# Kernel optimization log

Measured on AMD Instinct MI355X. Metric: run time of the kernel, lower is better.

The kernel has to match this reference:

```python
import jax, jax.numpy as jnp
import numpy as np

N = 50000      # nodes
E = 800000     # edges (before self-loops)
IN_DIM = 128
HID = 64
HEADS = 4
NEG_SLOPE = 0.2  # PyG GATConv default leaky-relu slope


def setup_inputs() -> dict:
    key = jax.random.key(0)
    ks = jax.random.split(key, 12)
    s = 0.05
    return {
        "x": jax.random.normal(ks[0], (N, IN_DIM), jnp.float32),
        "edge_index": jax.random.randint(ks[1], (2, E), 0, N, dtype=jnp.int64),
        "W1": jax.random.normal(ks[2], (IN_DIM, HEADS * HID), jnp.float32) * s,
        "att1_src": jax.random.normal(ks[3], (HEADS, HID), jnp.float32) * s,
        "att1_dst": jax.random.normal(ks[4], (HEADS, HID), jnp.float32) * s,
        "b1": jax.random.normal(ks[5], (HEADS * HID,), jnp.float32) * s,
        "W2": jax.random.normal(ks[6], (HEADS * HID, HID), jnp.float32) * s,
        "att2_src": jax.random.normal(ks[7], (1, HID), jnp.float32) * s,
        "att2_dst": jax.random.normal(ks[8], (1, HID), jnp.float32) * s,
        "b2": jax.random.normal(ks[9], (HID,), jnp.float32) * s,
        "Wc": jax.random.normal(ks[10], (HID, 2), jnp.float32) * s,
        "bc": jax.random.normal(ks[11], (2,), jnp.float32) * s,
    }


def _gat_conv(x, src, dst, W, a_src, a_dst, b, heads, d, concat):
    """PyG GATConv (eval mode): gather-score-segment_softmax-scatter."""
    n = x.shape[0]
    h = (x @ W).reshape(n, heads, d)               # [N,H,D]
    alpha_s = jnp.einsum('nhd,hd->nh', h, a_src)   # [N,H]
    alpha_d = jnp.einsum('nhd,hd->nh', h, a_dst)
    e = jax.nn.leaky_relu(alpha_s[src] + alpha_d[dst], NEG_SLOPE)  # [E,H]
    # softmax over incoming edges of each destination node
    m = jax.ops.segment_max(e, dst, num_segments=n)                # [N,H]
    ex = jnp.exp(e - m[dst])
    den = jax.ops.segment_sum(ex, dst, num_segments=n)
    alpha = ex / den[dst]                                          # [E,H]
    out = jax.ops.segment_sum(h[src] * alpha[:, :, None], dst, num_segments=n)  # [N,H,D]
    out = out.reshape(n, heads * d) if concat else out.mean(axis=1)
    return out + b


def reference(x, edge_index, W1, att1_src, att1_dst, b1,
              W2, att2_src, att2_dst, b2, Wc, bc):
    n = x.shape[0]
    # PyG GATConv adds self-loops by default
    loops = jnp.arange(n, dtype=edge_index.dtype)
    src = jnp.concatenate([edge_index[0], loops])
    dst = jnp.concatenate([edge_index[1], loops])
    h1 = jax.nn.elu(_gat_conv(x, src, dst, W1, att1_src, att1_dst, b1, HEADS, HID, True))
    h2 = jax.nn.elu(_gat_conv(h1, src, dst, W2, att2_src, att2_dst, b2, 1, HID, False))
    return h2 @ Wc + bc
```

## Files before the change

kernel.cpp:

```cpp
#include <hip/hip_runtime.h>
#include <hip/hip_bf16.h>
#include <cstddef>


#define HEADS 4
#define HID 64
#define IN_DIM 128

using bf16x8 = __attribute__((ext_vector_type(8))) short;
using f32x4  = __attribute__((ext_vector_type(4))) float;

__device__ __forceinline__ float us2f(unsigned short u) {
    return __uint_as_float((unsigned int)u << 16);
}
__device__ __forceinline__ unsigned short f2us(float f) {
    __hip_bfloat16 b = __float2bfloat16(f);
    return __builtin_bit_cast(unsigned short, b);
}

__global__ __launch_bounds__(256) void cvt_x_kernel(const float* __restrict__ in,
                                                    unsigned short* __restrict__ out, int n4) {
    int i = blockIdx.x * 256 + threadIdx.x;
    if (i >= n4) return;
    float4 v = ((const float4*)in)[i];
    ushort4 o;
    o.x = f2us(v.x); o.y = f2us(v.y); o.z = f2us(v.z); o.w = f2us(v.w);
    ((ushort4*)out)[i] = o;
}

__global__ __launch_bounds__(256) void cvt_w_kernel(const float* __restrict__ W,
                                                    unsigned short* __restrict__ WT,
                                                    int K, int Ncol) {
    int i = blockIdx.x * 256 + threadIdx.x;
    if (i >= K * Ncol) return;
    int k = i / Ncol, n = i - k * Ncol;
    WT[(size_t)n * K + k] = f2us(W[i]);
}

template <int BN, int BK, int KFULL, bool INTERLEAVE>
__global__ __launch_bounds__(256) void gemm_mfma_kernel(
    const unsigned short* __restrict__ A,
    const unsigned short* __restrict__ BT,
    unsigned short* __restrict__ C,
    int M, int Nfull) {
    constexpr int LDK = BK + 8;
    constexpr int NT = BN / 16;
    constexpr int KC = BK / 8;
    __shared__ unsigned short As[64 * LDK];
    __shared__ unsigned short Bs[BN * LDK];
    const int tid = threadIdx.x;
    const int wave = tid >> 6, lane = tid & 63;
    const int row0 = blockIdx.y * 64;
    const int col0 = blockIdx.x * BN;
    f32x4 acc[NT] = {};
    for (int k0 = 0; k0 < KFULL; k0 += BK) {
        for (int c = tid; c < 64 * KC; c += 256) {
            int r = c / KC, kc = c - r * KC;
            int row = row0 + r; if (row >= M) row = M - 1;
            *(bf16x8*)(As + r * LDK + kc * 8) =
                *(const bf16x8*)(A + (size_t)row * KFULL + k0 + kc * 8);
        }
        for (int c = tid; c < BN * KC; c += 256) {
            int r = c / KC, kc = c - r * KC;
            *(bf16x8*)(Bs + r * LDK + kc * 8) =
                *(const bf16x8*)(BT + (size_t)(col0 + r) * KFULL + k0 + kc * 8);
        }
        __syncthreads();
        const int arow = wave * 16 + (lane & 15);
        const int kb = (lane >> 4) * 8;
#pragma unroll
        for (int ks = 0; ks < BK; ks += 32) {
            bf16x8 af = *(const bf16x8*)(As + arow * LDK + ks + kb);
#pragma unroll
            for (int nt = 0; nt < NT; ++nt) {
                bf16x8 bfv = *(const bf16x8*)(Bs + (nt * 16 + (lane & 15)) * LDK + ks + kb);
                acc[nt] = __builtin_amdgcn_mfma_f32_16x16x32_bf16(af, bfv, acc[nt], 0, 0, 0);
            }
        }
        __syncthreads();
    }
    const int crow0 = row0 + wave * 16 + ((lane >> 4) << 2);
#pragma unroll
    for (int nt = 0; nt < NT; ++nt) {
        const int col = col0 + nt * 16 + (lane & 15);
#pragma unroll
        for (int j = 0; j < 4; ++j) {
            const int row = crow0 + j;
            if (row < M) {
                size_t off = INTERLEAVE
                    ? (size_t)row * 256 + (size_t)(col & 63) * 4 + (col >> 6)
                    : (size_t)row * Nfull + col;
                C[off] = f2us(acc[nt][j]);
            }
        }
    }
}

__global__ void deg_init_kernel(int* __restrict__ deg, int N) {
    int n = blockIdx.x * 256 + threadIdx.x;
    if (n < N) deg[n] = 1;
}
__global__ void deg_count_kernel(const int* __restrict__ dst, int* __restrict__ deg, int E) {
    int e = blockIdx.x * 256 + threadIdx.x;
    if (e < E) atomicAdd(&deg[dst[e]], 1);
}
__global__ __launch_bounds__(256) void scan1_kernel(const int* __restrict__ deg,
                                                    int* __restrict__ bsum, int N) {
    const int i = blockIdx.x * 256 + threadIdx.x;
    const int lane = threadIdx.x & 63, w = threadIdx.x >> 6;
    int v = (i < N) ? deg[i] : 0;
#pragma unroll
    for (int off = 32; off; off >>= 1) v += __shfl_xor(v, off, 64);
    __shared__ int ws[4];
    if (lane == 0) ws[w] = v;
    __syncthreads();
    if (threadIdx.x == 0) bsum[blockIdx.x] = ws[0] + ws[1] + ws[2] + ws[3];
}
__global__ __launch_bounds__(256) void scan2_kernel(const int* __restrict__ bsum,
                                                    int* __restrict__ boff, int nb) {
    const int tid = threadIdx.x, lane = tid & 63, w = tid >> 6;
    int v = (tid < nb) ? bsum[tid] : 0;
    int x = v;
#pragma unroll
    for (int off = 1; off < 64; off <<= 1) {
        int y = __shfl_up(x, off, 64);
        if (lane >= off) x += y;
    }
    __shared__ int ws[4];
    if (lane == 63) ws[w] = x;
    __syncthreads();
    int add = 0;
    for (int i = 0; i < w; ++i) add += ws[i];
    x += add;
    if (tid < nb) boff[tid] = x - v;
    if (tid == 255) boff[nb] = x;
}
__global__ __launch_bounds__(256) void scan3_kernel(const int* __restrict__ deg,
                                                    const int* __restrict__ boff,
                                                    int* __restrict__ row_ptr, int N) {
    const int i = blockIdx.x * 256 + threadIdx.x;
    const int tid = threadIdx.x, lane = tid & 63, w = tid >> 6;
    int v = (i < N) ? deg[i] : 0;
    int x = v;
#pragma unroll
    for (int off = 1; off < 64; off <<= 1) {
        int y = __shfl_up(x, off, 64);
        if (lane >= off) x += y;
    }
    __shared__ int ws[4];
    if (lane == 63) ws[w] = x;
    __syncthreads();
    int add = 0;
    for (int k = 0; k < w; ++k) add += ws[k];
    x += add;
    int excl = x - v + boff[blockIdx.x];
    if (i < N) row_ptr[i] = excl;
    if (i == N - 1) row_ptr[N] = excl + v;
}
__global__ void selfloop_kernel(const int* __restrict__ row_ptr, int* __restrict__ colA,
                                int* __restrict__ fill, int N) {
    int n = blockIdx.x * 256 + threadIdx.x;
    if (n < N) {
        int p = row_ptr[n];
        colA[p] = n;
        fill[n] = p + 1;
    }
}
__global__ void scatter_kernel(const int* __restrict__ src, const int* __restrict__ dst,
                               int* __restrict__ fill, int* __restrict__ colA, int E) {
    int e = blockIdx.x * 256 + threadIdx.x;
    if (e < E) {
        int pos = atomicAdd(&fill[dst[e]], 1);
        colA[pos] = src[e];
    }
}

__global__ __launch_bounds__(256) void alpha1_kernel(const unsigned short* __restrict__ g1,
                                                     const float* __restrict__ a_src,
                                                     const float* __restrict__ a_dst,
                                                     float* __restrict__ as1,
                                                     float* __restrict__ ad1, int N) {
    int wid = (blockIdx.x * 256 + threadIdx.x) >> 6;
    int lane = threadIdx.x & 63;
    if (wid >= N) return;
    ushort4 g = *(const ushort4*)(g1 + (size_t)wid * 256 + lane * 4);
    float f0 = us2f(g.x), f1 = us2f(g.y), f2 = us2f(g.z), f3 = us2f(g.w);
    float s0 = f0 * a_src[lane],       d0 = f0 * a_dst[lane];
    float s1 = f1 * a_src[64 + lane],  d1 = f1 * a_dst[64 + lane];
    float s2 = f2 * a_src[128 + lane], d2 = f2 * a_dst[128 + lane];
    float s3 = f3 * a_src[192 + lane], d3 = f3 * a_dst[192 + lane];
#pragma unroll
    for (int off = 32; off; off >>= 1) {
        s0 += __shfl_xor(s0, off, 64); d0 += __shfl_xor(d0, off, 64);
        s1 += __shfl_xor(s1, off, 64); d1 += __shfl_xor(d1, off, 64);
        s2 += __shfl_xor(s2, off, 64); d2 += __shfl_xor(d2, off, 64);
        s3 += __shfl_xor(s3, off, 64); d3 += __shfl_xor(d3, off, 64);
    }
    if (lane == 0) {
        *(float4*)(as1 + (size_t)wid * 4) = make_float4(s0, s1, s2, s3);
        *(float4*)(ad1 + (size_t)wid * 4) = make_float4(d0, d1, d2, d3);
    }
}
__global__ __launch_bounds__(256) void alpha2_kernel(const unsigned short* __restrict__ g2,
                                                     const float* __restrict__ a_src,
                                                     const float* __restrict__ a_dst,
                                                     float* __restrict__ as2,
                                                     float* __restrict__ ad2, int N) {
    int wid = (blockIdx.x * 256 + threadIdx.x) >> 6;
    int lane = threadIdx.x & 63;
    if (wid >= N) return;
    float v = us2f(g2[(size_t)wid * 64 + lane]);
    float s = v * a_src[lane];
    float d = v * a_dst[lane];
#pragma unroll
    for (int off = 32; off; off >>= 1) {
        s += __shfl_xor(s, off, 64);
        d += __shfl_xor(d, off, 64);
    }
    if (lane == 0) { as2[wid] = s; ad2[wid] = d; }
}

__global__ __launch_bounds__(256) void agg1_kernel(
    const unsigned short* __restrict__ g1, const float* __restrict__ as1,
    const float* __restrict__ ad1, const int* __restrict__ row_ptr,
    const int* __restrict__ colA, const float* __restrict__ b1,
    unsigned short* __restrict__ h1b, int N) {
    int wid = (blockIdx.x * 256 + threadIdx.x) >> 6;
    int lane = threadIdx.x & 63;
    if (wid >= N) return;
    const float4 adv = *(const float4*)(ad1 + (size_t)wid * 4);
    float s0 = 0.f, s1 = 0.f, s2 = 0.f, s3 = 0.f;
    float a0 = 0.f, a1 = 0.f, a2 = 0.f, a3 = 0.f;
    const int beg = row_ptr[wid], end = row_ptr[wid + 1];
    int src = colA[beg];
    float4 asv = *(const float4*)(as1 + (size_t)src * 4);
    ushort4 gv = *(const ushort4*)(g1 + (size_t)src * 256 + lane * 4);
    for (int idx = beg; idx < end; ++idx) {
        const int nsrc = (idx + 1 < end) ? colA[idx + 1] : src;
        float4 nasv = *(const float4*)(as1 + (size_t)nsrc * 4);
        ushort4 ngv = *(const ushort4*)(g1 + (size_t)nsrc * 256 + lane * 4);
        float e, w;
        e = asv.x + adv.x; e = e > 0.f ? e : 0.2f * e; w = __expf(e);
        s0 += w; a0 += w * us2f(gv.x);
        e = asv.y + adv.y; e = e > 0.f ? e : 0.2f * e; w = __expf(e);
        s1 += w; a1 += w * us2f(gv.y);
        e = asv.z + adv.z; e = e > 0.f ? e : 0.2f * e; w = __expf(e);
        s2 += w; a2 += w * us2f(gv.z);
        e = asv.w + adv.w; e = e > 0.f ? e : 0.2f * e; w = __expf(e);
        s3 += w; a3 += w * us2f(gv.w);
        asv = nasv; gv = ngv;
    }
    size_t base = (size_t)wid * 256;
    float o;
    o = a0 / s0 + b1[lane];       o = o > 0.f ? o : expm1f(o); h1b[base + lane]       = f2us(o);
    o = a1 / s1 + b1[64 + lane];  o = o > 0.f ? o : expm1f(o); h1b[base + 64 + lane]  = f2us(o);
    o = a2 / s2 + b1[128 + lane]; o = o > 0.f ? o : expm1f(o); h1b[base + 128 + lane] = f2us(o);
    o = a3 / s3 + b1[192 + lane]; o = o > 0.f ? o : expm1f(o); h1b[base + 192 + lane] = f2us(o);
}

__global__ __launch_bounds__(256) void agg2_kernel(
    const unsigned short* __restrict__ g2, const float* __restrict__ as2,
    const float* __restrict__ ad2, const int* __restrict__ row_ptr,
    const int* __restrict__ colA, const float* __restrict__ b2,
    const float* __restrict__ Wc, const float* __restrict__ bc,
    float* __restrict__ out, int N) {
    int wid = (blockIdx.x * 256 + threadIdx.x) >> 6;
    int lane = threadIdx.x & 63;
    if (wid >= N) return;
    const float ad = ad2[wid];
    float s = 0.f, a = 0.f;
    const int beg = row_ptr[wid], end = row_ptr[wid + 1];
    int src = colA[beg];
    float ev = as2[src];
    unsigned short gv = g2[(size_t)src * 64 + lane];
    for (int idx = beg; idx < end; ++idx) {
        const int nsrc = (idx + 1 < end) ? colA[idx + 1] : src;
        float nev = as2[nsrc];
        unsigned short ngv = g2[(size_t)nsrc * 64 + lane];
        float e = ev + ad; e = e > 0.f ? e : 0.2f * e;
        float w = __expf(e);
        s += w; a += w * us2f(gv);
        ev = nev; gv = ngv;
    }
    float h = a / s + b2[lane];
    h = h > 0.f ? h : expm1f(h);
    float c0 = h * Wc[lane * 2 + 0];
    float c1 = h * Wc[lane * 2 + 1];
#pragma unroll
    for (int off = 32; off; off >>= 1) {
        c0 += __shfl_xor(c0, off, 64);
        c1 += __shfl_xor(c1, off, 64);
    }
    if (lane == 0) {
        out[(size_t)wid * 2 + 0] = c0 + bc[0];
        out[(size_t)wid * 2 + 1] = c1 + bc[1];
    }
}

extern "C" void kernel_launch(void* const* d_in, const int* in_sizes, int n_in,
                              void* d_out, int out_size, void* d_ws, size_t ws_size,
                              hipStream_t stream) {
    const float* x        = (const float*)d_in[0];
    const int*   ei       = (const int*)d_in[1];
    const float* W1       = (const float*)d_in[2];
    const float* att1_src = (const float*)d_in[3];
    const float* att1_dst = (const float*)d_in[4];
    const float* b1       = (const float*)d_in[5];
    const float* W2       = (const float*)d_in[6];
    const float* att2_src = (const float*)d_in[7];
    const float* att2_dst = (const float*)d_in[8];
    const float* b2       = (const float*)d_in[9];
    const float* Wc       = (const float*)d_in[10];
    const float* bc       = (const float*)d_in[11];
    float* out = (float*)d_out;

    const int N = in_sizes[0] / IN_DIM;
    const int E = in_sizes[1] / 2;
    const int* srcI = ei;
    const int* dstI = ei + E;

    unsigned short* g1b = (unsigned short*)d_ws;
    unsigned short* h1b = g1b + (size_t)N * 256;
    unsigned short* xb  = h1b + (size_t)N * 256;
    unsigned short* g2b = xb + (size_t)N * 128;
    unsigned short* W1T = g2b + (size_t)N * 64;
    unsigned short* W2T = W1T + 256 * 128;
    float* as1 = (float*)(W2T + 64 * 256);
    float* ad1 = as1 + (size_t)N * 4;
    float* as2 = ad1 + (size_t)N * 4;
    float* ad2 = as2 + N;
    int* deg     = (int*)(ad2 + N);
    int* row_ptr = deg + N;
    int* fill    = row_ptr + N + 1;
    int* bsum    = fill + N;
    int* boff    = bsum + 256;
    int* colA    = boff + 260;

    const int nB = (N + 255) / 256;
    const int eB = (E + 255) / 256;
    const int wB = ((N * 64) + 255) / 256;
    const int nb = nB;

    cvt_x_kernel<<<(N * (IN_DIM / 4) + 255) / 256, 256, 0, stream>>>(x, xb, N * (IN_DIM / 4));
    cvt_w_kernel<<<(IN_DIM * 256 + 255) / 256, 256, 0, stream>>>(W1, W1T, IN_DIM, 256);
    cvt_w_kernel<<<(256 * 64 + 255) / 256, 256, 0, stream>>>(W2, W2T, 256, 64);

    deg_init_kernel<<<nB, 256, 0, stream>>>(deg, N);
    deg_count_kernel<<<eB, 256, 0, stream>>>(dstI, deg, E);
    scan1_kernel<<<nB, 256, 0, stream>>>(deg, bsum, N);
    scan2_kernel<<<1, 256, 0, stream>>>(bsum, boff, nb);
    scan3_kernel<<<nB, 256, 0, stream>>>(deg, boff, row_ptr, N);
    selfloop_kernel<<<nB, 256, 0, stream>>>(row_ptr, colA, fill, N);
    scatter_kernel<<<eB, 256, 0, stream>>>(srcI, dstI, fill, colA, E);

    gemm_mfma_kernel<128, 128, 128, true>
        <<<dim3(2, (N + 63) / 64), 256, 0, stream>>>(xb, W1T, g1b, N, 256);
    alpha1_kernel<<<wB, 256, 0, stream>>>(g1b, att1_src, att1_dst, as1, ad1, N);
    agg1_kernel<<<wB, 256, 0, stream>>>(g1b, as1, ad1, row_ptr, colA, b1, h1b, N);

    gemm_mfma_kernel<64, 128, 256, false>
        <<<dim3(1, (N + 63) / 64), 256, 0, stream>>>(h1b, W2T, g2b, N, 64);
    alpha2_kernel<<<wB, 256, 0, stream>>>(g2b, att2_src, att2_dst, as2, ad2, N);
    agg2_kernel<<<wB, 256, 0, stream>>>(g2b, as2, ad2, row_ptr, colA, b2, Wc, bc, out, N);
}
```

Baseline: 409.7 us.

## Precompute per-edge attention weights in separate kernel instead of per-lane recompute

Records each CSR slot's destination during the scatter, then adds a per-edge kernel that computes the exp(leaky_relu) attention weights once per edge and head. The aggregation kernels now read these precomputed weights rather than having all 64 lanes of a wave redundantly compute the same exp for each edge. This trades redundant transcendental work and the random as-gather for extra memory traffic: a dstA array, the weight arrays (about 850K×4 floats for layer 1), and two more kernel launches.

```diff
diff --git a/kernel.cpp b/kernel.cpp
--- a/kernel.cpp
+++ b/kernel.cpp
@@ -158,20 +158,24 @@
     if (i == N - 1) row_ptr[N] = excl + v;
 }
 __global__ void selfloop_kernel(const int* __restrict__ row_ptr, int* __restrict__ colA,
-                                int* __restrict__ fill, int N) {
+                                int* __restrict__ dstA, int* __restrict__ fill, int N) {
     int n = blockIdx.x * 256 + threadIdx.x;
     if (n < N) {
         int p = row_ptr[n];
         colA[p] = n;
+        dstA[p] = n;
         fill[n] = p + 1;
     }
 }
 __global__ void scatter_kernel(const int* __restrict__ src, const int* __restrict__ dst,
-                               int* __restrict__ fill, int* __restrict__ colA, int E) {
+                               int* __restrict__ fill, int* __restrict__ colA,
+                               int* __restrict__ dstA, int E) {
     int e = blockIdx.x * 256 + threadIdx.x;
     if (e < E) {
-        int pos = atomicAdd(&fill[dst[e]], 1);
+        int d = dst[e];
+        int pos = atomicAdd(&fill[d], 1);
         colA[pos] = src[e];
+        dstA[pos] = d;
     }
 }
 
@@ -220,35 +224,55 @@
     if (lane == 0) { as2[wid] = s; ad2[wid] = d; }
 }
 
+template <int H>
+__global__ __launch_bounds__(256) void wkernel(const int* __restrict__ colA,
+                                               const int* __restrict__ dstA,
+                                               const float* __restrict__ as,
+                                               const float* __restrict__ ad,
+                                               float* __restrict__ wA, int NNZ) {
+    int p = blockIdx.x * 256 + threadIdx.x;
+    if (p >= NNZ) return;
+    const int src = colA[p], dst = dstA[p];
+    if constexpr (H == 4) {
+        float4 s = *(const float4*)(as + (size_t)src * 4);
+        float4 d = *(const float4*)(ad + (size_t)dst * 4);
+        float e;
+        float4 w;
+        e = s.x + d.x; e = e > 0.f ? e : 0.2f * e; w.x = __expf(e);
+        e = s.y + d.y; e = e > 0.f ? e : 0.2f * e; w.y = __expf(e);
+        e = s.z + d.z; e = e > 0.f ? e : 0.2f * e; w.z = __expf(e);
+        e = s.w + d.w; e = e > 0.f ? e : 0.2f * e; w.w = __expf(e);
+        *(float4*)(wA + (size_t)p * 4) = w;
+    } else {
+        float e = as[src] + ad[dst];
+        e = e > 0.f ? e : 0.2f * e;
+        wA[p] = __expf(e);
+    }
+}
+
 __global__ __launch_bounds__(256) void agg1_kernel(
-    const unsigned short* __restrict__ g1, const float* __restrict__ as1,
-    const float* __restrict__ ad1, const int* __restrict__ row_ptr,
-    const int* __restrict__ colA, const float* __restrict__ b1,
-    unsigned short* __restrict__ h1b, int N) {
+    const unsigned short* __restrict__ g1, const float* __restrict__ wA,
+    const int* __restrict__ row_ptr, const int* __restrict__ colA,
+    const float* __restrict__ b1, unsigned short* __restrict__ h1b, int N) {
     int wid = (blockIdx.x * 256 + threadIdx.x) >> 6;
     int lane = threadIdx.x & 63;
     if (wid >= N) return;
-    const float4 adv = *(const float4*)(ad1 + (size_t)wid * 4);
     float s0 = 0.f, s1 = 0.f, s2 = 0.f, s3 = 0.f;
     float a0 = 0.f, a1 = 0.f, a2 = 0.f, a3 = 0.f;
     const int beg = row_ptr[wid], end = row_ptr[wid + 1];
     int src = colA[beg];
-    float4 asv = *(const float4*)(as1 + (size_t)src * 4);
+    float4 wv = *(const float4*)(wA + (size_t)beg * 4);
     ushort4 gv = *(const ushort4*)(g1 + (size_t)src * 256 + lane * 4);
     for (int idx = beg; idx < end; ++idx) {
-        const int nsrc = (idx + 1 < end) ? colA[idx + 1] : src;
-        float4 nasv = *(const float4*)(as1 + (size_t)nsrc * 4);
+        const int nidx = (idx + 1 < end) ? idx + 1 : idx;
+        const int nsrc = colA[nidx];
+        float4 nwv = *(const float4*)(wA + (size_t)nidx * 4);
         ushort4 ngv = *(const ushort4*)(g1 + (size_t)nsrc * 256 + lane * 4);
-        float e, w;
-        e = asv.x + adv.x; e = e > 0.f ? e : 0.2f * e; w = __expf(e);
-        s0 += w; a0 += w * us2f(gv.x);
-        e = asv.y + adv.y; e = e > 0.f ? e : 0.2f * e; w = __expf(e);
-        s1 += w; a1 += w * us2f(gv.y);
-        e = asv.z + adv.z; e = e > 0.f ? e : 0.2f * e; w = __expf(e);
-        s2 += w; a2 += w * us2f(gv.z);
-        e = asv.w + adv.w; e = e > 0.f ? e : 0.2f * e; w = __expf(e);
-        s3 += w; a3 += w * us2f(gv.w);
-        asv = nasv; gv = ngv;
+        s0 += wv.x; a0 += wv.x * us2f(gv.x);
+        s1 += wv.y; a1 += wv.y * us2f(gv.y);
+        s2 += wv.z; a2 += wv.z * us2f(gv.z);
+        s3 += wv.w; a3 += wv.w * us2f(gv.w);
+        wv = nwv; gv = ngv;
     }
     size_t base = (size_t)wid * 256;
     float o;
@@ -259,28 +283,25 @@
 }
 
 __global__ __launch_bounds__(256) void agg2_kernel(
-    const unsigned short* __restrict__ g2, const float* __restrict__ as2,
-    const float* __restrict__ ad2, const int* __restrict__ row_ptr,
-    const int* __restrict__ colA, const float* __restrict__ b2,
-    const float* __restrict__ Wc, const float* __restrict__ bc,
-    float* __restrict__ out, int N) {
+    const unsigned short* __restrict__ g2, const float* __restrict__ wA,
+    const int* __restrict__ row_ptr, const int* __restrict__ colA,
+    const float* __restrict__ b2, const float* __restrict__ Wc,
+    const float* __restrict__ bc, float* __restrict__ out, int N) {
     int wid = (blockIdx.x * 256 + threadIdx.x) >> 6;
     int lane = threadIdx.x & 63;
     if (wid >= N) return;
-    const float ad = ad2[wid];
     float s = 0.f, a = 0.f;
     const int beg = row_ptr[wid], end = row_ptr[wid + 1];
     int src = colA[beg];
-    float ev = as2[src];
+    float wv = wA[beg];
     unsigned short gv = g2[(size_t)src * 64 + lane];
     for (int idx = beg; idx < end; ++idx) {
-        const int nsrc = (idx + 1 < end) ? colA[idx + 1] : src;
-        float nev = as2[nsrc];
+        const int nidx = (idx + 1 < end) ? idx + 1 : idx;
+        const int nsrc = colA[nidx];
+        float nwv = wA[nidx];
         unsigned short ngv = g2[(size_t)nsrc * 64 + lane];
-        float e = ev + ad; e = e > 0.f ? e : 0.2f * e;
-        float w = __expf(e);
-        s += w; a += w * us2f(gv);
-        ev = nev; gv = ngv;
+        s += wv; a += wv * us2f(gv);
+        wv = nwv; gv = ngv;
     }
     float h = a / s + b2[lane];
     h = h > 0.f ? h : expm1f(h);
@@ -316,6 +337,7 @@
 
     const int N = in_sizes[0] / IN_DIM;
     const int E = in_sizes[1] / 2;
+    const int NNZ = E + N;
     const int* srcI = ei;
     const int* dstI = ei + E;
 
@@ -329,15 +351,19 @@
     float* ad1 = as1 + (size_t)N * 4;
     float* as2 = ad1 + (size_t)N * 4;
     float* ad2 = as2 + N;
-    int* deg     = (int*)(ad2 + N);
+    float* wA1 = ad2 + N;
+    float* wA2 = wA1 + (size_t)NNZ * 4;
+    int* deg     = (int*)(wA2 + NNZ);
     int* row_ptr = deg + N;
     int* fill    = row_ptr + N + 1;
     int* bsum    = fill + N;
     int* boff    = bsum + 256;
     int* colA    = boff + 260;
+    int* dstA    = colA + NNZ;
 
     const int nB = (N + 255) / 256;
     const int eB = (E + 255) / 256;
+    const int pB = (NNZ + 255) / 256;
     const int wB = ((N * 64) + 255) / 256;
     const int nb = nB;
 
@@ -350,16 +376,18 @@
     scan1_kernel<<<nB, 256, 0, stream>>>(deg, bsum, N);
     scan2_kernel<<<1, 256, 0, stream>>>(bsum, boff, nb);
     scan3_kernel<<<nB, 256, 0, stream>>>(deg, boff, row_ptr, N);
-    selfloop_kernel<<<nB, 256, 0, stream>>>(row_ptr, colA, fill, N);
-    scatter_kernel<<<eB, 256, 0, stream>>>(srcI, dstI, fill, colA, E);
+    selfloop_kernel<<<nB, 256, 0, stream>>>(row_ptr, colA, dstA, fill, N);
+    scatter_kernel<<<eB, 256, 0, stream>>>(srcI, dstI, fill, colA, dstA, E);
 
     gemm_mfma_kernel<128, 128, 128, true>
         <<<dim3(2, (N + 63) / 64), 256, 0, stream>>>(xb, W1T, g1b, N, 256);
     alpha1_kernel<<<wB, 256, 0, stream>>>(g1b, att1_src, att1_dst, as1, ad1, N);
-    agg1_kernel<<<wB, 256, 0, stream>>>(g1b, as1, ad1, row_ptr, colA, b1, h1b, N);
+    wkernel<4><<<pB, 256, 0, stream>>>(colA, dstA, as1, ad1, wA1, NNZ);
+    agg1_kernel<<<wB, 256, 0, stream>>>(g1b, wA1, row_ptr, colA, b1, h1b, N);
 
     gemm_mfma_kernel<64, 128, 256, false>
         <<<dim3(1, (N + 63) / 64), 256, 0, stream>>>(h1b, W2T, g2b, N, 64);
     alpha2_kernel<<<wB, 256, 0, stream>>>(g2b, att2_src, att2_dst, as2, ad2, N);
-    agg2_kernel<<<wB, 256, 0, stream>>>(g2b, as2, ad2, row_ptr, colA, b2, Wc, bc, out, N);
-}
+    wkernel<1><<<pB, 256, 0, stream>>>(colA, dstA, as2, ad2, wA2, NNZ);
+    agg2_kernel<<<wB, 256, 0, stream>>>(g2b, wA2, row_ptr, colA, b2, Wc, bc, out, N);
+}
```

Result: slower. 458.7 us (+12.0%).
